# Kernel optimization log

Measured on AMD Instinct MI355X. Metric: run time of the kernel, lower is better.

Reference implementation:

```python
import jax, jax.numpy as jnp
import numpy as np

V, H, HALF, B, L = 32000, 256, 128, 64, 512


def setup_inputs() -> dict:
    key = jax.random.key(0)
    ks = jax.random.split(key, 16)
    s = 0.02
    return {
        "seq": jax.random.randint(ks[0], (B, L), 0, V),
        "embed": jax.random.normal(ks[1], (V, H), jnp.float32) * s,
        "W1": jax.random.normal(ks[2], (H, 2 * H), jnp.float32) * s,
        "b1": jnp.zeros((2 * H,), jnp.float32),
        "W2": jax.random.normal(ks[3], (2 * H, H), jnp.float32) * s,
        "b2": jnp.zeros((H,), jnp.float32),
        "ln_g": jnp.ones((H,), jnp.float32),
        "ln_b": jnp.zeros((H,), jnp.float32),
        "Wsem": jax.random.normal(ks[4], (H, HALF), jnp.float32) * s,
        "bsem": jnp.zeros((HALF,), jnp.float32),
        "Wepi": jax.random.normal(ks[5], (H, HALF), jnp.float32) * s,
        "bepi": jnp.zeros((HALF,), jnp.float32),
        "Wout": jax.random.normal(ks[6], (2 * HALF, V), jnp.float32) * s,
        "bout": jnp.zeros((V,), jnp.float32),
    }


def _encode(seq, embed, W1, b1, W2, b2, ln_g, ln_b):
    e = embed[seq]                                  # [B, L, H]
    ff = jnp.maximum(e @ W1 + b1, 0.0) @ W2 + b2    # [B, L, H]
    x = e + ff
    mu = jnp.mean(x, -1, keepdims=True)
    var = jnp.mean((x - mu) ** 2, -1, keepdims=True)
    return (x - mu) / jnp.sqrt(var + 1e-5) * ln_g + ln_b


def _delta_step(carry, inp):
    M_s, M_e = carry
    ks, ke, scale = inp  # ks/ke: [B, half]; scale scalar
    vps = jnp.einsum("bij,bj->bi", M_s, ks)
    dvs = ks - vps / (jnp.sum(ks * ks, -1, keepdims=True) + 1e-6)
    M_s = M_s + dvs[:, :, None] * ks[:, None, :]
    vpe = jnp.einsum("bij,bj->bi", M_e, ke)
    dve = ke - vpe / (jnp.sum(ke * ke, -1, keepdims=True) + 1e-6)
    M_e = M_e + scale * (dve[:, :, None] * ke[:, None, :])
    return (M_s, M_e), None


def reference(seq, embed, W1, b1, W2, b2, ln_g, ln_b,
              Wsem, bsem, Wepi, bepi, Wout, bout):
    h = _encode(seq, embed, W1, b1, W2, b2, ln_g, ln_b)   # [B, L, H]
    Bs, Ls, _ = h.shape
    half = Wsem.shape[1]
    # keys for all write steps t = 0 .. L-2, precomputed in one GEMM
    ks_all = (h[:, :-1] @ Wsem + bsem).transpose(1, 0, 2)  # [L-1, B, half]
    ke_all = (h[:, :-1] @ Wepi + bepi).transpose(1, 0, 2)
    scales = jnp.arange(1, Ls, dtype=h.dtype) / Ls         # (t+1)/L
    M0 = jnp.zeros((Bs, half, half), h.dtype)
    (M_s, M_e), _ = jax.lax.scan(_delta_step, (M0, M0), (ks_all, ke_all, scales))
    q = h[:, -1, :]
    cs = jnp.einsum("bij,bj->bi", M_s, q @ Wsem + bsem)
    ce = jnp.einsum("bij,bj->bi", M_e, q @ Wepi + bepi)
    return jnp.concatenate([cs, ce], -1) @ Wout + bout     # [B, V]
```

## Files before the change

kernel.cpp:

```cpp
#include <hip/hip_runtime.h>
#include <hip/hip_bf16.h>
#include <stdint.h>

#define B_   64
#define L_   512
#define H_   256
#define H2_  512
#define HALF_ 128
#define V_   32000
#define NTOK_ (B_*L_)

typedef __attribute__((ext_vector_type(8))) short bf16x8;
typedef __attribute__((ext_vector_type(4))) float f32x4;

__device__ __forceinline__ float bf2f(short h){
    union { unsigned u; float f; } v; v.u = ((unsigned)(unsigned short)h) << 16; return v.f;
}
__device__ __forceinline__ short f2bf(float f){
    union { float f; unsigned u; } v; v.f = f;
    unsigned r = v.u + 0x7fffu + ((v.u >> 16) & 1u);
    return (short)(r >> 16);
}

__global__ __launch_bounds__(256) void k_prep(
    const float* __restrict__ W1, const float* __restrict__ W2,
    const float* __restrict__ Wsem, const float* __restrict__ Wepi,
    const float* __restrict__ bsem, const float* __restrict__ bepi,
    short* __restrict__ W1t, short* __restrict__ W2t, short* __restrict__ Wpt,
    float* __restrict__ bp)
{
    const int n = blockIdx.x, t = threadIdx.x;
    if (n < 512) {
        W1t[n*256 + t] = f2bf(W1[t*H2_ + n]);
    } else if (n < 768) {
        const int r = n - 512;
        W2t[r*512 + t]       = f2bf(W2[t*H_ + r]);
        W2t[r*512 + t + 256] = f2bf(W2[(t+256)*H_ + r]);
    } else {
        const int r = n - 768;
        Wpt[r*256 + t] = f2bf(r < 128 ? Wsem[t*HALF_ + r] : Wepi[t*HALF_ + (r-128)]);
        if (t == 0) bp[r] = (r < 128) ? bsem[r] : bepi[r-128];
    }
}

#define EA_LD 264

__global__ __launch_bounds__(512, 4) void k_encode_fused(
    const int* __restrict__ seq, const float* __restrict__ embed,
    const short* __restrict__ W1t, const float* __restrict__ b1,
    const short* __restrict__ W2t, const float* __restrict__ b2,
    const float* __restrict__ ln_g, const float* __restrict__ ln_b,
    const short* __restrict__ Wpt, const float* __restrict__ bp,
    float* __restrict__ kske)
{
    __shared__ __align__(16) short eA[64*EA_LD];
    __shared__ __align__(16) short fB[64*EA_LD];
    __shared__ float2 lnp[8][64];
    __shared__ float2 stat[64];

    const int tid = threadIdx.x;
    const int lo  = tid & 15;
    const int hi  = (tid >> 4) & 3;
    const int wv  = tid >> 6;
    const int n0  = wv * 32;
    const int tokBase = blockIdx.x * 64;
    short* hA = eA;

    {
        const int tk = tid >> 3, part = tid & 7;
        const float4* src = (const float4*)(embed + (size_t)seq[tokBase + tk] * H_);
#pragma unroll
        for (int i = 0; i < 8; ++i) {
            float4 v = src[part + 8*i];
            short4 o; o.x = f2bf(v.x); o.y = f2bf(v.y); o.z = f2bf(v.z); o.w = f2bf(v.w);
            *(short4*)&eA[tk*EA_LD + (part + 8*i)*4] = o;
        }
    }
    __syncthreads();

    f32x4 acc2[4][2];
#pragma unroll
    for (int m = 0; m < 4; ++m) { acc2[m][0] = (f32x4){0,0,0,0}; acc2[m][1] = (f32x4){0,0,0,0}; }

    for (int h = 0; h < 2; ++h) {
        f32x4 acc1[4][2];
#pragma unroll
        for (int m = 0; m < 4; ++m) { acc1[m][0] = (f32x4){0,0,0,0}; acc1[m][1] = (f32x4){0,0,0,0}; }
        {
            const short* Bb = W1t + ((size_t)(h*256 + n0 + lo))*256;
            bf16x8 bc0 = *(const bf16x8*)(Bb + 8*hi);
            bf16x8 bc1 = *(const bf16x8*)(Bb + 16*256 + 8*hi);
#pragma unroll
            for (int kk = 0; kk < 8; ++kk) {
                const int k0 = kk*32 + 8*hi;
                bf16x8 bn0, bn1;
                if (kk < 7) {
                    bn0 = *(const bf16x8*)(Bb + k0 + 32);
                    bn1 = *(const bf16x8*)(Bb + 16*256 + k0 + 32);
                }
#pragma unroll
                for (int m = 0; m < 4; ++m) {
                    bf16x8 a = *(const bf16x8*)&eA[(lo + 16*m)*EA_LD + k0];
                    acc1[m][0] = __builtin_amdgcn_mfma_f32_16x16x32_bf16(a, bc0, acc1[m][0], 0,0,0);
                    acc1[m][1] = __builtin_amdgcn_mfma_f32_16x16x32_bf16(a, bc1, acc1[m][1], 0,0,0);
                }
                if (kk < 7) { bc0 = bn0; bc1 = bn1; }
            }
        }
        {
            const float bb0 = b1[h*256 + n0 + lo];
            const float bb1 = b1[h*256 + n0 + 16 + lo];
#pragma unroll
            for (int m = 0; m < 4; ++m)
#pragma unroll
                for (int r = 0; r < 4; ++r) {
                    const int row = m*16 + hi*4 + r;
                    fB[row*EA_LD + n0 + lo]      = f2bf(fmaxf(acc1[m][0][r] + bb0, 0.f));
                    fB[row*EA_LD + n0 + 16 + lo] = f2bf(fmaxf(acc1[m][1][r] + bb1, 0.f));
                }
        }
        __syncthreads();
        {
            const short* Bb = W2t + ((size_t)(n0 + lo))*512 + h*256;
            bf16x8 bc0 = *(const bf16x8*)(Bb + 8*hi);
            bf16x8 bc1 = *(const bf16x8*)(Bb + 16*512 + 8*hi);
#pragma unroll
            for (int kk = 0; kk < 8; ++kk) {
                const int k0 = kk*32 + 8*hi;
                bf16x8 bn0, bn1;
                if (kk < 7) {
                    bn0 = *(const bf16x8*)(Bb + k0 + 32);
                    bn1 = *(const bf16x8*)(Bb + 16*512 + k0 + 32);
                }
#pragma unroll
                for (int m = 0; m < 4; ++m) {
                    bf16x8 a = *(const bf16x8*)&fB[(lo + 16*m)*EA_LD + k0];
                    acc2[m][0] = __builtin_amdgcn_mfma_f32_16x16x32_bf16(a, bc0, acc2[m][0], 0,0,0);
                    acc2[m][1] = __builtin_amdgcn_mfma_f32_16x16x32_bf16(a, bc1, acc2[m][1], 0,0,0);
                }
                if (kk < 7) { bc0 = bn0; bc1 = bn1; }
            }
        }
        __syncthreads();
    }

    const int col0 = n0 + lo, col1 = n0 + 16 + lo;

    {
        const float bb0 = b2[col0], bb1 = b2[col1];
#pragma unroll
        for (int m = 0; m < 4; ++m)
#pragma unroll
            for (int r = 0; r < 4; ++r) {
                const int row = m*16 + hi*4 + r;
                acc2[m][0][r] += bb0 + bf2f(eA[row*EA_LD + col0]);
                acc2[m][1][r] += bb1 + bf2f(eA[row*EA_LD + col1]);
            }
#pragma unroll
        for (int m = 0; m < 4; ++m)
#pragma unroll
            for (int r = 0; r < 4; ++r) {
                float x0 = acc2[m][0][r], x1 = acc2[m][1][r];
                float s  = x0 + x1;
                float s2 = fmaf(x0, x0, x1*x1);
#pragma unroll
                for (int o = 1; o < 16; o <<= 1) { s += __shfl_xor(s, o, 64); s2 += __shfl_xor(s2, o, 64); }
                if (lo == 0) { float2 p; p.x = s; p.y = s2; lnp[wv][m*16 + hi*4 + r] = p; }
            }
    }
    __syncthreads();
    if (tid < 64) {
        float s = 0.f, s2 = 0.f;
#pragma unroll
        for (int w = 0; w < 8; ++w) { float2 p = lnp[w][tid]; s += p.x; s2 += p.y; }
        float mu  = s * (1.f/256.f);
        float var = s2 * (1.f/256.f) - mu*mu;
        float2 st; st.x = mu; st.y = rsqrtf(var + 1e-5f);
        stat[tid] = st;
    }
    __syncthreads();

    {
        const float g0 = ln_g[col0], g1 = ln_g[col1];
        const float be0 = ln_b[col0], be1 = ln_b[col1];
#pragma unroll
        for (int m = 0; m < 4; ++m)
#pragma unroll
            for (int r = 0; r < 4; ++r) {
                const int row = m*16 + hi*4 + r;
                float2 st = stat[row];
                hA[row*EA_LD + col0] = f2bf((acc2[m][0][r] - st.x) * st.y * g0 + be0);
                hA[row*EA_LD + col1] = f2bf((acc2[m][1][r] - st.x) * st.y * g1 + be1);
            }
    }
    __syncthreads();

    f32x4 acc3[4][2];
#pragma unroll
    for (int m = 0; m < 4; ++m) { acc3[m][0] = (f32x4){0,0,0,0}; acc3[m][1] = (f32x4){0,0,0,0}; }
    {
        const short* Bb = Wpt + ((size_t)(n0 + lo))*256;
        bf16x8 bc0 = *(const bf16x8*)(Bb + 8*hi);
        bf16x8 bc1 = *(const bf16x8*)(Bb + 16*256 + 8*hi);
#pragma unroll
        for (int kk = 0; kk < 8; ++kk) {
            const int k0 = kk*32 + 8*hi;
            bf16x8 bn0, bn1;
            if (kk < 7) {
                bn0 = *(const bf16x8*)(Bb + k0 + 32);
                bn1 = *(const bf16x8*)(Bb + 16*256 + k0 + 32);
            }
#pragma unroll
            for (int m = 0; m < 4; ++m) {
                bf16x8 a = *(const bf16x8*)&hA[(lo + 16*m)*EA_LD + k0];
                acc3[m][0] = __builtin_amdgcn_mfma_f32_16x16x32_bf16(a, bc0, acc3[m][0], 0,0,0);
                acc3[m][1] = __builtin_amdgcn_mfma_f32_16x16x32_bf16(a, bc1, acc3[m][1], 0,0,0);
            }
            if (kk < 7) { bc0 = bn0; bc1 = bn1; }
        }
    }
    {
        const float bp0 = bp[col0], bp1 = bp[col1];
#pragma unroll
        for (int m = 0; m < 4; ++m)
#pragma unroll
            for (int r = 0; r < 4; ++r) {
                const int row = m*16 + hi*4 + r;
                kske[(size_t)(tokBase + row)*256 + col0] = acc3[m][0][r] + bp0;
                kske[(size_t)(tokBase + row)*256 + col1] = acc3[m][1][r] + bp1;
            }
    }
}

#define SCAN_BODY(CC, GA, KXA, KYA, NGA, GB, KXB, KYB, NGB) do {              \
    const int c_ = (CC);                                                      \
    wls[2*l] = w.x; wls[2*l+1] = w.y;                                         \
    float p0=0.f, p1=0.f, p2=0.f, p3=0.f;                                     \
    _Pragma("unroll")                                                         \
    for (int i = 0; i < 8; ++i) {                                             \
        float4 wv2 = *(const float4*)&wls[q*32 + 4*i];                        \
        p0 = fmaf(kq[i].x, wv2.x, p0); p1 = fmaf(kq[i].y, wv2.y, p1);         \
        p2 = fmaf(kq[i].z, wv2.z, p2); p3 = fmaf(kq[i].w, wv2.w, p3);         \
    }                                                                         \
    float bb = (p0 + p1) + (p2 + p3);                                         \
    bb += __shfl_xor(bb, 16, 64);                                             \
    bb += __shfl_xor(bb, 32, 64);                                             \
    if (c_ > 0) {                                                             \
        const float* krow = kb + ((size_t)((c_-1)*16 + lo))*256 + q*32;       \
        _Pragma("unroll")                                                     \
        for (int i = 0; i < 8; ++i) kq[i] = *(const float4*)(krow + 4*i);     \
        const float* gr = &Gs[(c_-1)*256 + lo*16];                            \
        _Pragma("unroll")                                                     \
        for (int i = 0; i < 4; ++i) {                                         \
            float4 gt = *(const float4*)(gr + 4*i);                           \
            GB[4*i]=gt.x; GB[4*i+1]=gt.y; GB[4*i+2]=gt.z; GB[4*i+3]=gt.w;     \
        }                                                                     \
        NGB = gvs[(c_-1)*16 + lo];                                            \
        const float* kdr = kb + ((size_t)((c_-1)*16))*256 + 2*l;              \
        _Pragma("unroll")                                                     \
        for (int j = 0; j < 16; ++j) {                                        \
            float2 kt = *(const float2*)(kdr + (size_t)j*256);                \
            KXB[j] = kt.x; KYB[j] = kt.y;                                     \
        }                                                                     \
    }                                                                         \
    const int tl_ = c_*16 + lo;                                               \
    const float cl_ = chain ? ((tl_ < 511) ? (float)(tl_+1)*(1.f/512.f) : 0.f)\
                            : ((tl_ < 511) ? 1.f : 0.f);                      \
    _Pragma("unroll")                                                         \
    for (int j = 15; j >= 0; --j) {                                           \
        float dj = __int_as_float(__builtin_amdgcn_readlane(__float_as_int(bb), j)); \
        bb = fmaf(dj, GA[j], bb);                                             \
        float tg = NGA * dj;                                                  \
        float tc = cl_ * dj;                                                  \
        float gd = __int_as_float(__builtin_amdgcn_readlane(__float_as_int(tg), j)); \
        float cd = __int_as_float(__builtin_amdgcn_readlane(__float_as_int(tc), j)); \
        w.x = fmaf(gd, KXA[j], w.x);  w.y = fmaf(gd, KYA[j], w.y);            \
        ax  = fmaf(cd, KXA[j], ax);   ay  = fmaf(cd, KYA[j], ay);             \
    }                                                                         \
} while (0)

__global__ __launch_bounds__(256) void k_scan(
    const float* __restrict__ kske, float* __restrict__ cvec)
{
    __shared__ float Gs[32*256];
    __shared__ float gvs[32*16];
    __shared__ float wls[128];

    const int b = blockIdx.x, chain = blockIdx.y;
    const int tid = threadIdx.x;
    const int wvi = tid >> 6;
    const int l   = tid & 63;
    const int lo  = l & 15, q = l >> 4;
    const float* kb = kske + ((size_t)b*L_)*256 + chain*HALF_;

    for (int cc = 0; cc < 8; ++cc) {
        const int c = wvi*8 + cc;
        const float* rowp = kb + ((size_t)(c*16 + lo))*256 + 8*q;
        bf16x8 ah[4], al[4];
#pragma unroll
        for (int m = 0; m < 4; ++m) {
            float4 v0 = *(const float4*)(rowp + m*32);
            float4 v1 = *(const float4*)(rowp + m*32 + 4);
            float f[8] = {v0.x,v0.y,v0.z,v0.w,v1.x,v1.y,v1.z,v1.w};
#pragma unroll
            for (int i = 0; i < 8; ++i) {
                short hh = f2bf(f[i]);
                ah[m][i] = hh;
                al[m][i] = f2bf(f[i] - bf2f(hh));
            }
        }
        f32x4 g = {0.f,0.f,0.f,0.f};
#pragma unroll
        for (int m = 0; m < 4; ++m) {
            g = __builtin_amdgcn_mfma_f32_16x16x32_bf16(ah[m], ah[m], g, 0,0,0);
            g = __builtin_amdgcn_mfma_f32_16x16x32_bf16(ah[m], al[m], g, 0,0,0);
            g = __builtin_amdgcn_mfma_f32_16x16x32_bf16(al[m], ah[m], g, 0,0,0);
        }
        float cand = (lo & 2) ? ((lo & 1) ? g[3] : g[2]) : ((lo & 1) ? g[1] : g[0]);
        float dval = __shfl(cand, (lo >> 2)*16 + lo, 64);

        const int tcol = c*16 + lo;
        float beta = 1.f / (dval + 1e-6f);
        float gam  = chain ? ((float)(tcol+1) * (1.f/512.f)) * beta : beta;
        if (tcol == 511) gam = 0.f;
#pragma unroll
        for (int r = 0; r < 4; ++r)
            Gs[c*256 + (4*q + r)*16 + lo] = -gam * g[r];
        if (l < 16) gvs[c*16 + lo] = -gam;
    }
    __syncthreads();
    if (wvi != 0) return;

    float2 w = *(const float2*)(kb + (size_t)511*256 + 2*l);
    float ax = 0.f, ay = 0.f;

    float ga[16], kxa[16], kya[16], nga;
    float gb_[16], kxb[16], kyb[16], ngb;
    float4 kq[8];

    {
        const float* krow = kb + ((size_t)(31*16 + lo))*256 + q*32;
#pragma unroll
        for (int i = 0; i < 8; ++i) kq[i] = *(const float4*)(krow + 4*i);
        const float* gr = &Gs[31*256 + lo*16];
#pragma unroll
        for (int i = 0; i < 4; ++i) {
            float4 gt = *(const float4*)(gr + 4*i);
            ga[4*i]=gt.x; ga[4*i+1]=gt.y; ga[4*i+2]=gt.z; ga[4*i+3]=gt.w;
        }
        nga = gvs[31*16 + lo];
        const float* kdr = kb + ((size_t)(31*16))*256 + 2*l;
#pragma unroll
        for (int j = 0; j < 16; ++j) {
            float2 kt = *(const float2*)(kdr + (size_t)j*256);
            kxa[j] = kt.x; kya[j] = kt.y;
        }
    }

    for (int it = 0; it < 16; ++it) {
        SCAN_BODY(31 - 2*it, ga,  kxa, kya, nga, gb_, kxb, kyb, ngb);
        SCAN_BODY(30 - 2*it, gb_, kxb, kyb, ngb, ga,  kxa, kya, nga);
    }

    float2 outv; outv.x = ax; outv.y = ay;
    *(float2*)(cvec + b*256 + chain*HALF_ + 2*l) = outv;
}

__global__ __launch_bounds__(512) void k_out(
    const float* __restrict__ cvec, const float* __restrict__ Wout,
    const float* __restrict__ bout, float* __restrict__ out)
{
    __shared__ float c_s[64][256];
    const int t = threadIdx.x;
    {
        float* flat = &c_s[0][0];
#pragma unroll
        for (int r = 0; r < 32; ++r) flat[t + r*512] = cvec[t + r*512];
    }
    __syncthreads();

    const int col = blockIdx.x * 128 + (t & 63) * 2;
    const int bg  = (t >> 6) * 8;
    float accx[8], accy[8];
#pragma unroll
    for (int i = 0; i < 8; ++i) { accx[i] = 0.f; accy[i] = 0.f; }

#pragma unroll 8
    for (int i = 0; i < 256; ++i) {
        float2 wv = *(const float2*)&Wout[(size_t)i*V_ + col];
#pragma unroll
        for (int bb = 0; bb < 8; ++bb) {
            float cv = c_s[bg + bb][i];
            accx[bb] = fmaf(cv, wv.x, accx[bb]);
            accy[bb] = fmaf(cv, wv.y, accy[bb]);
        }
    }
    const float bo0 = bout[col], bo1 = bout[col+1];
#pragma unroll
    for (int bb = 0; bb < 8; ++bb) {
        float2 o; o.x = accx[bb] + bo0; o.y = accy[bb] + bo1;
        *(float2*)&out[(size_t)(bg + bb)*V_ + col] = o;
    }
}

extern "C" void kernel_launch(void* const* d_in, const int* in_sizes, int n_in,
                              void* d_out, int out_size, void* d_ws, size_t ws_size,
                              hipStream_t stream)
{
    (void)in_sizes; (void)n_in; (void)out_size; (void)ws_size;
    const int*   seq   = (const int*)  d_in[0];
    const float* embed = (const float*)d_in[1];
    const float* W1    = (const float*)d_in[2];
    const float* b1    = (const float*)d_in[3];
    const float* W2    = (const float*)d_in[4];
    const float* b2    = (const float*)d_in[5];
    const float* ln_g  = (const float*)d_in[6];
    const float* ln_b  = (const float*)d_in[7];
    const float* Wsem  = (const float*)d_in[8];
    const float* bsem  = (const float*)d_in[9];
    const float* Wepi  = (const float*)d_in[10];
    const float* bepi  = (const float*)d_in[11];
    const float* Wout  = (const float*)d_in[12];
    const float* bout  = (const float*)d_in[13];
    float* out = (float*)d_out;

    char* wp = (char*)d_ws;
    short* W1t = (short*)wp;  wp += (size_t)512*256*2;
    short* W2t = (short*)wp;  wp += (size_t)256*512*2;
    short* Wpt = (short*)wp;  wp += (size_t)256*256*2;
    float* bp  = (float*)wp;  wp += 256*4;
    float* kske= (float*)wp;  wp += (size_t)NTOK_*256*4;
    float* cvec= (float*)wp;

    k_prep<<<1024, 256, 0, stream>>>(W1, W2, Wsem, Wepi, bsem, bepi, W1t, W2t, Wpt, bp);
    k_encode_fused<<<NTOK_/64, 512, 0, stream>>>(seq, embed, W1t, b1, W2t, b2,
                                                 ln_g, ln_b, Wpt, bp, kske);
    k_scan<<<dim3(B_, 2), 256, 0, stream>>>(kske, cvec);
    k_out<<<V_/128, 512, 0, stream>>>(cvec, Wout, bout, out);
}
```

Measured before the change: 118.5 us.

## Run output projection on MFMA with split-bf16 (hi/lo) three-term product

```diff
diff --git a/kernel.cpp b/kernel.cpp
--- a/kernel.cpp
+++ b/kernel.cpp
@@ -280,7 +280,7 @@
 } while (0)
 
 __global__ __launch_bounds__(256) void k_scan(
-    const float* __restrict__ kske, float* __restrict__ cvec)
+    const float* __restrict__ kske, short* __restrict__ chi, short* __restrict__ clo)
 {
     __shared__ float Gs[32*256];
     __shared__ float gvs[32*16];
@@ -362,45 +362,71 @@
         SCAN_BODY(30 - 2*it, gb_, kxb, kyb, ngb, ga,  kxa, kya, nga);
     }
 
-    float2 outv; outv.x = ax; outv.y = ay;
-    *(float2*)(cvec + b*256 + chain*HALF_ + 2*l) = outv;
-}
-
-__global__ __launch_bounds__(512) void k_out(
-    const float* __restrict__ cvec, const float* __restrict__ Wout,
-    const float* __restrict__ bout, float* __restrict__ out)
+    short2 hv, lv;
+    hv.x = f2bf(ax); lv.x = f2bf(ax - bf2f(hv.x));
+    hv.y = f2bf(ay); lv.y = f2bf(ay - bf2f(hv.y));
+    *(short2*)&chi[b*256 + chain*HALF_ + 2*l] = hv;
+    *(short2*)&clo[b*256 + chain*HALF_ + 2*l] = lv;
+}
+
+__global__ __launch_bounds__(256) void k_out(
+    const short* __restrict__ chi, const short* __restrict__ clo,
+    const float* __restrict__ Wout, const float* __restrict__ bout,
+    float* __restrict__ out)
 {
-    __shared__ float c_s[64][256];
-    const int t = threadIdx.x;
-    {
-        float* flat = &c_s[0][0];
-#pragma unroll
-        for (int r = 0; r < 32; ++r) flat[t + r*512] = cvec[t + r*512];
-    }
-    __syncthreads();
-
-    const int col = blockIdx.x * 128 + (t & 63) * 2;
-    const int bg  = (t >> 6) * 8;
-    float accx[8], accy[8];
-#pragma unroll
-    for (int i = 0; i < 8; ++i) { accx[i] = 0.f; accy[i] = 0.f; }
-
-#pragma unroll 8
-    for (int i = 0; i < 256; ++i) {
-        float2 wv = *(const float2*)&Wout[(size_t)i*V_ + col];
-#pragma unroll
-        for (int bb = 0; bb < 8; ++bb) {
-            float cv = c_s[bg + bb][i];
-            accx[bb] = fmaf(cv, wv.x, accx[bb]);
-            accy[bb] = fmaf(cv, wv.y, accy[bb]);
-        }
-    }
-    const float bo0 = bout[col], bo1 = bout[col+1];
-#pragma unroll
-    for (int bb = 0; bb < 8; ++bb) {
-        float2 o; o.x = accx[bb] + bo0; o.y = accy[bb] + bo1;
-        *(float2*)&out[(size_t)(bg + bb)*V_ + col] = o;
-    }
+    __shared__ __align__(16) short ch_s[64*EA_LD];
+    __shared__ __align__(16) short cl_s[64*EA_LD];
+    const int t  = threadIdx.x;
+    const int lo = t & 15;
+    const int hi = (t >> 4) & 3;
+    const int wv = t >> 6;
+
+    {
+        const int4* sh = (const int4*)chi;
+        const int4* sl = (const int4*)clo;
+#pragma unroll
+        for (int i = 0; i < 8; ++i) {
+            const int idx = t + 256*i;
+            const int row = idx >> 5;
+            const int c8  = (idx & 31) * 8;
+            *(int4*)&ch_s[row*EA_LD + c8] = sh[idx];
+            *(int4*)&cl_s[row*EA_LD + c8] = sl[idx];
+        }
+    }
+    __syncthreads();
+
+    const int colbase = blockIdx.x * 64 + wv * 16;
+    f32x4 acc[4];
+#pragma unroll
+    for (int m = 0; m < 4; ++m) acc[m] = (f32x4){0.f,0.f,0.f,0.f};
+
+#pragma unroll
+    for (int kk = 0; kk < 8; ++kk) {
+        const int k0 = kk*32 + 8*hi;
+        bf16x8 bh, bl;
+#pragma unroll
+        for (int i = 0; i < 8; ++i) {
+            float wf = Wout[(size_t)(k0 + i)*V_ + colbase + lo];
+            short wh = f2bf(wf);
+            bh[i] = wh;
+            bl[i] = f2bf(wf - bf2f(wh));
+        }
+#pragma unroll
+        for (int m = 0; m < 4; ++m) {
+            bf16x8 ah = *(const bf16x8*)&ch_s[(m*16 + lo)*EA_LD + k0];
+            bf16x8 al = *(const bf16x8*)&cl_s[(m*16 + lo)*EA_LD + k0];
+            acc[m] = __builtin_amdgcn_mfma_f32_16x16x32_bf16(ah, bh, acc[m], 0,0,0);
+            acc[m] = __builtin_amdgcn_mfma_f32_16x16x32_bf16(ah, bl, acc[m], 0,0,0);
+            acc[m] = __builtin_amdgcn_mfma_f32_16x16x32_bf16(al, bh, acc[m], 0,0,0);
+        }
+    }
+
+    const float bo = bout[colbase + lo];
+#pragma unroll
+    for (int m = 0; m < 4; ++m)
+#pragma unroll
+        for (int r = 0; r < 4; ++r)
+            out[(size_t)(m*16 + hi*4 + r)*V_ + colbase + lo] = acc[m][r] + bo;
 }
 
 extern "C" void kernel_launch(void* const* d_in, const int* in_sizes, int n_in,
@@ -430,11 +456,12 @@
     short* Wpt = (short*)wp;  wp += (size_t)256*256*2;
     float* bp  = (float*)wp;  wp += 256*4;
     float* kske= (float*)wp;  wp += (size_t)NTOK_*256*4;
-    float* cvec= (float*)wp;
+    short* chi = (short*)wp;  wp += (size_t)B_*256*2;
+    short* clo = (short*)wp;  wp += (size_t)B_*256*2;
 
     k_prep<<<1024, 256, 0, stream>>>(W1, W2, Wsem, Wepi, bsem, bepi, W1t, W2t, Wpt, bp);
     k_encode_fused<<<NTOK_/64, 512, 0, stream>>>(seq, embed, W1t, b1, W2t, b2,
                                                  ln_g, ln_b, Wpt, bp, kske);
-    k_scan<<<dim3(B_, 2), 256, 0, stream>>>(kske, cvec);
-    k_out<<<V_/128, 512, 0, stream>>>(cvec, Wout, bout, out);
-}
+    k_scan<<<dim3(B_, 2), 256, 0, stream>>>(kske, chi, clo);
+    k_out<<<V_/64, 256, 0, stream>>>(chi, clo, Wout, bout, out);
+}
```

Result: faster. 104.0 us, median of 2 (-12.2%).
